# Kernel tuning notes

Hardware: AMD Instinct MI355X
Metric: run time of the kernel (lower is better)

The kernel has to match this reference:

```python
import jax, jax.numpy as jnp
import numpy as np

N_NODES = 100000
N_EDGES = 500000
D = 256
EPS = 0.1  # GIN epsilon applied on self-loop relation


def setup_inputs() -> dict:
    key = jax.random.key(0)
    ks = jax.random.split(key, 9)
    return {
        "x": jax.random.normal(ks[0], (N_NODES, D), dtype=jnp.float32),
        "W_self": jax.random.normal(ks[1], (D, D), dtype=jnp.float32) * 0.05,
        "W_r1": jax.random.normal(ks[2], (D, D), dtype=jnp.float32) * 0.05,
        "W_r2": jax.random.normal(ks[3], (D, D), dtype=jnp.float32) * 0.05,
        "bias": jax.random.normal(ks[4], (D,), dtype=jnp.float32) * 0.05,
        "src1": jax.random.randint(ks[5], (N_EDGES,), 0, N_NODES, dtype=jnp.int32),
        "dst1": jax.random.randint(ks[6], (N_EDGES,), 0, N_NODES, dtype=jnp.int32),
        "src2": jax.random.randint(ks[7], (N_EDGES,), 0, N_NODES, dtype=jnp.int32),
        "dst2": jax.random.randint(ks[8], (N_EDGES,), 0, N_NODES, dtype=jnp.int32),
    }


def reference(x, W_self, W_r1, W_r2, bias, src1, dst1, src2, dst2):
    # self-loop relation: features scaled by (1+eps); one self-loop edge per node
    # so copy_u + sum delivers each node exactly its own message.
    h = (1.0 + EPS) * (x @ W_self)
    # regular relations: per-node message = x @ W, gathered along src edges,
    # scatter-summed at dst (DGL fn.copy_u + fn.sum, cross-etype 'sum' reducer).
    msg1 = x @ W_r1
    h = h + jax.ops.segment_sum(msg1[src1], dst1, num_segments=N_NODES)
    msg2 = x @ W_r2
    h = h + jax.ops.segment_sum(msg2[src2], dst2, num_segments=N_NODES)
    # bias + activation, then second activation (applied twice in original);
    # mlp/batch_norm are None, dropout is identity in eval.
    h = jax.nn.relu(h + bias)
    h = jax.nn.relu(h)
    return h
```

## Files before the change

kernel.cpp:

```cpp
#include <hip/hip_runtime.h>

#define N_NODES 100000
#define N_EDGES 500000
#define D 256
#define CAP 32

typedef __bf16 bf16x8 __attribute__((ext_vector_type(8)));
typedef float  f32x4  __attribute__((ext_vector_type(4)));
typedef unsigned int u32x2 __attribute__((ext_vector_type(2)));

#define GLDS(gp, lp) \
    __builtin_amdgcn_global_load_lds((const __attribute__((address_space(1))) void*)(gp), \
                                     (__attribute__((address_space(3))) void*)(lp), 16, 0, 0)

__device__ __forceinline__ unsigned short f2bf(float f) {
    unsigned int u = __float_as_uint(f);
    u += 0x7fffu + ((u >> 16) & 1u);
    return (unsigned short)(u >> 16);
}
__device__ __forceinline__ float bf2f(unsigned short b) {
    return __uint_as_float(((unsigned int)b) << 16);
}

#define PREP_BLOCKS 17188

__global__ __launch_bounds__(256) void prep_kernel(
    const float* __restrict__ x, unsigned short* __restrict__ xb,
    const float* __restrict__ Ws, const float* __restrict__ W1,
    const float* __restrict__ W2, unsigned short* __restrict__ Wt,
    const int* __restrict__ src1, const int* __restrict__ dst1,
    const int* __restrict__ src2, const int* __restrict__ dst2,
    int* __restrict__ cnt1, int* __restrict__ cnt2,
    int* __restrict__ bkt1, int* __restrict__ bkt2)
{
    const int wid  = blockIdx.x * 4 + (threadIdx.x >> 6);
    const int lane = threadIdx.x & 63;
    const int group = wid / 22;
    const int pos   = wid - group * 22;

    if (pos < 16) {
        int cw = group * 16 + pos;
        if (cw >= 50000) return;
        size_t i = (size_t)cw * 512 + (size_t)lane * 8;
        float4 a = *(const float4*)(x + i);
        float4 c = *(const float4*)(x + i + 4);
        union { unsigned short s[8]; uint4 u; } o;
        o.s[0] = f2bf(a.x); o.s[1] = f2bf(a.y); o.s[2] = f2bf(a.z); o.s[3] = f2bf(a.w);
        o.s[4] = f2bf(c.x); o.s[5] = f2bf(c.y); o.s[6] = f2bf(c.z); o.s[7] = f2bf(c.w);
        *(uint4*)(xb + i) = o.u;
    } else if (pos < 21) {
        int bw = group * 5 + (pos - 16);
        int e = bw * 64 + lane;
        if (e >= 2 * N_EDGES) return;
        bool r2 = (e >= N_EDGES);
        const int* src = r2 ? src2 : src1;
        const int* dst = r2 ? dst2 : dst1;
        int* cnt = r2 ? cnt2 : cnt1;
        int* bkt = r2 ? bkt2 : bkt1;
        int ei = r2 ? e - N_EDGES : e;
        int s = src[ei], d = dst[ei];
        int p = atomicAdd(&cnt[d], 1);
        if (p < CAP) bkt[d * CAP + p] = s;
    } else {
        int idx = group * 64 + lane;
        if (idx >= 3 * D * D) return;
        int k = idx >> 8;
        int n = idx & (D - 1);
        const float* W = (k < D) ? Ws : (k < 2 * D ? W1 : W2);
        float scale = (k < D) ? 1.1f : 1.0f;
        Wt[(size_t)n * (3 * D) + k] = f2bf(W[(size_t)(k & (D - 1)) * D + n] * scale);
    }
}

__global__ __launch_bounds__(256) void gather_kernel(
    const unsigned short* __restrict__ xb,
    const int* __restrict__ cnt1, const int* __restrict__ cnt2,
    const int* __restrict__ bkt1, const int* __restrict__ bkt2,
    unsigned short* __restrict__ xa1, unsigned short* __restrict__ xa2)
{
    long long gid = (long long)blockIdx.x * blockDim.x + threadIdx.x;
    int w = (int)(gid >> 6);
    int lane = (int)(gid & 63);
    if (w >= 2 * N_NODES) return;
    int node = w >> 1;
    int rel  = w & 1;

    const int* cnt = rel ? cnt2 : cnt1;
    const int* bkt = rel ? bkt2 : bkt1;
    unsigned short* xa = rel ? xa2 : xa1;

    int c = cnt[node]; if (c > CAP) c = CAP;
    int sid = (lane < c) ? bkt[(size_t)node * CAP + lane] : 0;

    ushort4 v[8];
    #pragma unroll
    for (int t = 0; t < 8; ++t) {
        int s = __shfl(sid, t);
        v[t] = *(const ushort4*)(xb + (size_t)s * D + lane * 4);
    }

    float a0 = 0.f, a1 = 0.f, a2 = 0.f, a3 = 0.f;
    #pragma unroll
    for (int t = 0; t < 8; ++t) {
        if (t < c) {
            a0 += bf2f(v[t].x); a1 += bf2f(v[t].y);
            a2 += bf2f(v[t].z); a3 += bf2f(v[t].w);
        }
    }
    for (int e = 8; e < c; ++e) {
        int s = __shfl(sid, e);
        ushort4 t = *(const ushort4*)(xb + (size_t)s * D + lane * 4);
        a0 += bf2f(t.x); a1 += bf2f(t.y); a2 += bf2f(t.z); a3 += bf2f(t.w);
    }

    u32x2 o;
    o.x = (unsigned)f2bf(a0) | ((unsigned)f2bf(a1) << 16);
    o.y = (unsigned)f2bf(a2) | ((unsigned)f2bf(a3) << 16);
    __builtin_nontemporal_store(o, (u32x2*)(xa + (size_t)node * D + lane * 4));
}

__global__ __launch_bounds__(512) void gemm_kernel(
    const unsigned short* __restrict__ xb,
    const unsigned short* __restrict__ xa1,
    const unsigned short* __restrict__ xa2,
    const unsigned short* __restrict__ Wt,
    const float* __restrict__ bias, float* __restrict__ out)
{
    __shared__ unsigned short Alds[128 * 32];
    __shared__ unsigned short Blds[256 * 32];

    const int tid  = threadIdx.x;
    const int lane = tid & 63;
    const int wave = tid >> 6;
    const int quad = lane >> 4;
    const int l15  = lane & 15;
    const int m0 = blockIdx.x * 128;
    const int wm = (wave >> 2) * 64;
    const int wn = (wave & 3) * 64;

    const unsigned short* Aseg[3] = {xb, xa1, xa2};

    f32x4 acc[4][4] = {};

    for (int kt = 0; kt < 24; ++kt) {
        const int seg = kt >> 3;
        const int ko  = (kt & 7) * 32;
        const unsigned short* __restrict__ A = Aseg[seg];

        {
            int row = tid >> 2, kq = tid & 3;
            int m = m0 + row;
            if (m >= N_NODES) m = N_NODES - 1;
            GLDS(A + (size_t)m * D + ko + kq * 8, Alds + tid * 8);
        }
        {
            int n = tid >> 2, kq = tid & 3;
            GLDS(Wt + (size_t)n * (3 * D) + kt * 32 + kq * 8, Blds + tid * 8);
        }
        {
            int t2 = tid + 512;
            int n = t2 >> 2, kq = t2 & 3;
            GLDS(Wt + (size_t)n * (3 * D) + kt * 32 + kq * 8, Blds + t2 * 8);
        }
        __syncthreads();

        bf16x8 af[4], bfr[4];
        #pragma unroll
        for (int i = 0; i < 4; ++i) {
            af[i]  = *(const bf16x8*)(Alds + (wm + i * 16 + l15) * 32 + quad * 8);
            bfr[i] = *(const bf16x8*)(Blds + (wn + i * 16 + l15) * 32 + quad * 8);
        }
        #pragma unroll
        for (int i = 0; i < 4; ++i)
            #pragma unroll
            for (int j = 0; j < 4; ++j)
                acc[i][j] = __builtin_amdgcn_mfma_f32_16x16x32_bf16(
                    af[i], bfr[j], acc[i][j], 0, 0, 0);
        __syncthreads();
    }

    #pragma unroll
    for (int j = 0; j < 4; ++j) {
        int col = wn + j * 16 + l15;
        float bj = bias[col];
        #pragma unroll
        for (int i = 0; i < 4; ++i) {
            int rb = m0 + wm + i * 16 + quad * 4;
            #pragma unroll
            for (int r = 0; r < 4; ++r) {
                int m = rb + r;
                if (m < N_NODES)
                    __builtin_nontemporal_store(
                        fmaxf(acc[i][j][r] + bj, 0.f),
                        out + (size_t)m * D + col);
            }
        }
    }
}

extern "C" void kernel_launch(void* const* d_in, const int* in_sizes, int n_in,
                              void* d_out, int out_size, void* d_ws, size_t ws_size,
                              hipStream_t stream) {
    const float* x    = (const float*)d_in[0];
    const float* Ws   = (const float*)d_in[1];
    const float* W1   = (const float*)d_in[2];
    const float* W2   = (const float*)d_in[3];
    const float* bias = (const float*)d_in[4];
    const int* src1   = (const int*)d_in[5];
    const int* dst1   = (const int*)d_in[6];
    const int* src2   = (const int*)d_in[7];
    const int* dst2   = (const int*)d_in[8];
    float* out = (float*)d_out;

    char* p = (char*)d_ws;
    unsigned short* xb  = (unsigned short*)p; p += (size_t)N_NODES * D * 2;
    unsigned short* xa1 = (unsigned short*)p; p += (size_t)N_NODES * D * 2;
    unsigned short* xa2 = (unsigned short*)p; p += (size_t)N_NODES * D * 2;
    int* cnt1 = (int*)p; p += (size_t)N_NODES * 4;
    int* cnt2 = (int*)p; p += (size_t)N_NODES * 4;
    int* bkt1 = (int*)p; p += (size_t)N_NODES * CAP * 4;
    int* bkt2 = (int*)p; p += (size_t)N_NODES * CAP * 4;
    unsigned short* Wt = (unsigned short*)p;

    (void)hipMemsetAsync(cnt1, 0, (size_t)2 * N_NODES * 4, stream);

    prep_kernel<<<PREP_BLOCKS, 256, 0, stream>>>(
        x, xb, Ws, W1, W2, Wt, src1, dst1, src2, dst2, cnt1, cnt2, bkt1, bkt2);

    {
        long long total = (long long)2 * N_NODES * 64;
        gather_kernel<<<(int)((total + 255) / 256), 256, 0, stream>>>(
            xb, cnt1, cnt2, bkt1, bkt2, xa1, xa2);
    }
    {
        gemm_kernel<<<(N_NODES + 127) / 128, 512, 0, stream>>>(
            xb, xa1, xa2, Wt, bias, out);
    }
}
```

Measured before the change: 403.9 us.

## Register-prefetch GEMM tiles and XOR-swizzle LDS layout in gemm kernel

Replaces the direct global-to-LDS loads in the GEMM with register staging. The next K-tile is loaded into registers while the current tile is consumed by MFMAs, and the registers are written to LDS at the start of each iteration. LDS tiles are also XOR-swizzled on the 16-byte chunk index to cut bank conflicts on the fragment reads. This costs extra VGPRs and an explicit register-to-LDS store per tile. It still uses a single LDS buffer, so the two barriers per iteration remain.

Result: no change. 403.1 us (-0.2%).

```diff
diff --git a/kernel.cpp b/kernel.cpp
--- a/kernel.cpp
+++ b/kernel.cpp
@@ -8,10 +8,6 @@
 typedef __bf16 bf16x8 __attribute__((ext_vector_type(8)));
 typedef float  f32x4  __attribute__((ext_vector_type(4)));
 typedef unsigned int u32x2 __attribute__((ext_vector_type(2)));
-
-#define GLDS(gp, lp) \
-    __builtin_amdgcn_global_load_lds((const __attribute__((address_space(1))) void*)(gp), \
-                                     (__attribute__((address_space(3))) void*)(lp), 16, 0, 0)
 
 __device__ __forceinline__ unsigned short f2bf(float f) {
     unsigned int u = __float_as_uint(f);
@@ -140,35 +136,39 @@
 
     const unsigned short* Aseg[3] = {xb, xa1, xa2};
 
+    const int rowA = tid >> 2, kqA = tid & 3;
+    int mA = m0 + rowA; if (mA >= N_NODES) mA = N_NODES - 1;
+    const int wAoff  = rowA * 32 + ((kqA ^ ((rowA >> 1) & 3)) * 8);
+    const int nB0 = tid >> 2, nB1 = nB0 + 128;
+    const int wB0off = nB0 * 32 + ((kqA ^ ((nB0 >> 1) & 3)) * 8);
+    const int wB1off = nB1 * 32 + ((kqA ^ ((nB1 >> 1) & 3)) * 8);
+    const int swz = (l15 >> 1) & 3;
+
     f32x4 acc[4][4] = {};
 
+    uint4 ra  = *(const uint4*)(Aseg[0] + (size_t)mA * D + kqA * 8);
+    uint4 rb0 = *(const uint4*)(Wt + (size_t)nB0 * (3 * D) + kqA * 8);
+    uint4 rb1 = *(const uint4*)(Wt + (size_t)nB1 * (3 * D) + kqA * 8);
+
     for (int kt = 0; kt < 24; ++kt) {
-        const int seg = kt >> 3;
-        const int ko  = (kt & 7) * 32;
-        const unsigned short* __restrict__ A = Aseg[seg];
-
-        {
-            int row = tid >> 2, kq = tid & 3;
-            int m = m0 + row;
-            if (m >= N_NODES) m = N_NODES - 1;
-            GLDS(A + (size_t)m * D + ko + kq * 8, Alds + tid * 8);
-        }
-        {
-            int n = tid >> 2, kq = tid & 3;
-            GLDS(Wt + (size_t)n * (3 * D) + kt * 32 + kq * 8, Blds + tid * 8);
-        }
-        {
-            int t2 = tid + 512;
-            int n = t2 >> 2, kq = t2 & 3;
-            GLDS(Wt + (size_t)n * (3 * D) + kt * 32 + kq * 8, Blds + t2 * 8);
-        }
+        *(uint4*)(Alds + wAoff) = ra;
+        *(uint4*)(Blds + wB0off) = rb0;
+        *(uint4*)(Blds + wB1off) = rb1;
         __syncthreads();
+
+        if (kt + 1 < 24) {
+            const unsigned short* __restrict__ An = Aseg[(kt + 1) >> 3];
+            const int kon = ((kt + 1) & 7) * 32;
+            ra  = *(const uint4*)(An + (size_t)mA * D + kon + kqA * 8);
+            rb0 = *(const uint4*)(Wt + (size_t)nB0 * (3 * D) + (kt + 1) * 32 + kqA * 8);
+            rb1 = *(const uint4*)(Wt + (size_t)nB1 * (3 * D) + (kt + 1) * 32 + kqA * 8);
+        }
 
         bf16x8 af[4], bfr[4];
         #pragma unroll
         for (int i = 0; i < 4; ++i) {
-            af[i]  = *(const bf16x8*)(Alds + (wm + i * 16 + l15) * 32 + quad * 8);
-            bfr[i] = *(const bf16x8*)(Blds + (wn + i * 16 + l15) * 32 + quad * 8);
+            af[i]  = *(const bf16x8*)(Alds + (wm + i * 16 + l15) * 32 + ((quad ^ swz) * 8));
+            bfr[i] = *(const bf16x8*)(Blds + (wn + i * 16 + l15) * 32 + ((quad ^ swz) * 8));
         }
         #pragma unroll
         for (int i = 0; i < 4; ++i)
```

## Stage full-K A tile per segment in swizzled LDS, read B directly from global

Applied to the files above, without the earlier changes.

The GEMM kernel now loads a whole 128x256 A segment into LDS per relation, using an XOR swizzle to avoid bank conflicts. This cuts the number of barriers from 48 to 6 per block. B fragments are no longer staged in LDS; each wave loads its Wt fragments straight from global/L2 every k-step, relying on the small weight matrix being cache resident. This removes the per-k-tile sync and LDS traffic for B. In exchange it adds uncached-per-wave global loads on the MFMA critical path and a larger 64KB LDS footprint that may lower occupancy.

Result: slower. 474.0 us (+17.4%).

```diff
diff --git a/kernel.cpp b/kernel.cpp
--- a/kernel.cpp
+++ b/kernel.cpp
@@ -8,10 +8,6 @@
 typedef __bf16 bf16x8 __attribute__((ext_vector_type(8)));
 typedef float  f32x4  __attribute__((ext_vector_type(4)));
 typedef unsigned int u32x2 __attribute__((ext_vector_type(2)));
-
-#define GLDS(gp, lp) \
-    __builtin_amdgcn_global_load_lds((const __attribute__((address_space(1))) void*)(gp), \
-                                     (__attribute__((address_space(3))) void*)(lp), 16, 0, 0)
 
 __device__ __forceinline__ unsigned short f2bf(float f) {
     unsigned int u = __float_as_uint(f);
@@ -126,8 +122,7 @@
     const unsigned short* __restrict__ Wt,
     const float* __restrict__ bias, float* __restrict__ out)
 {
-    __shared__ unsigned short Alds[128 * 32];
-    __shared__ unsigned short Blds[256 * 32];
+    __shared__ unsigned short Alds[128 * 256];
 
     const int tid  = threadIdx.x;
     const int lane = tid & 63;
@@ -140,42 +135,48 @@
 
     const unsigned short* Aseg[3] = {xb, xa1, xa2};
 
+    int bbase[4];
+    #pragma unroll
+    for (int j = 0; j < 4; ++j)
+        bbase[j] = (wn + j * 16 + l15) * (3 * D) + quad * 8;
+
+    const int rowS = tid >> 5;
+    const int cS   = tid & 31;
+
     f32x4 acc[4][4] = {};
 
-    for (int kt = 0; kt < 24; ++kt) {
-        const int seg = kt >> 3;
-        const int ko  = (kt & 7) * 32;
+    for (int seg = 0; seg < 3; ++seg) {
         const unsigned short* __restrict__ A = Aseg[seg];
 
-        {
-            int row = tid >> 2, kq = tid & 3;
-            int m = m0 + row;
-            if (m >= N_NODES) m = N_NODES - 1;
-            GLDS(A + (size_t)m * D + ko + kq * 8, Alds + tid * 8);
-        }
-        {
-            int n = tid >> 2, kq = tid & 3;
-            GLDS(Wt + (size_t)n * (3 * D) + kt * 32 + kq * 8, Blds + tid * 8);
-        }
-        {
-            int t2 = tid + 512;
-            int n = t2 >> 2, kq = t2 & 3;
-            GLDS(Wt + (size_t)n * (3 * D) + kt * 32 + kq * 8, Blds + t2 * 8);
+        #pragma unroll
+        for (int s = 0; s < 8; ++s) {
+            int row = rowS + s * 16;
+            int m = m0 + row; if (m >= N_NODES) m = N_NODES - 1;
+            uint4 v = *(const uint4*)(A + (size_t)m * D + cS * 8);
+            *(uint4*)(Alds + row * 256 + ((cS ^ (row & 7)) * 8)) = v;
         }
         __syncthreads();
 
-        bf16x8 af[4], bfr[4];
         #pragma unroll
-        for (int i = 0; i < 4; ++i) {
-            af[i]  = *(const bf16x8*)(Alds + (wm + i * 16 + l15) * 32 + quad * 8);
-            bfr[i] = *(const bf16x8*)(Blds + (wn + i * 16 + l15) * 32 + quad * 8);
-        }
-        #pragma unroll
-        for (int i = 0; i < 4; ++i)
+        for (int kin = 0; kin < 8; ++kin) {
+            const int kt = seg * 8 + kin;
+            bf16x8 af[4], bfr[4];
+            #pragma unroll
+            for (int i = 0; i < 4; ++i) {
+                int row = wm + i * 16 + l15;
+                af[i] = *(const bf16x8*)(Alds + row * 256 +
+                                         (((kin * 4 + quad) ^ (row & 7)) * 8));
+            }
             #pragma unroll
             for (int j = 0; j < 4; ++j)
-                acc[i][j] = __builtin_amdgcn_mfma_f32_16x16x32_bf16(
-                    af[i], bfr[j], acc[i][j], 0, 0, 0);
+                bfr[j] = *(const bf16x8*)(Wt + bbase[j] + kt * 32);
+            #pragma unroll
+            for (int i = 0; i < 4; ++i)
+                #pragma unroll
+                for (int j = 0; j < 4; ++j)
+                    acc[i][j] = __builtin_amdgcn_mfma_f32_16x16x32_bf16(
+                        af[i], bfr[j], acc[i][j], 0, 0, 0);
+        }
         __syncthreads();
     }
 
```
